# Kernel tuning notes

Measured on AMD Instinct MI355X. Metric: run time of the kernel, lower is better.

The kernel has to match this reference:

```python
import jax, jax.numpy as jnp
import numpy as np

# Config (matches init_kwargs / input_specs)
H = 128      # hidden_dim
D = 3        # depth (atom message-passing steps)
L = 2        # layers (molecule readout steps)
N = 100000   # total nodes in batch
E = 400000   # total directed edges
G = 5000     # number of graphs (molecules)
FN = 64      # num_atom_type
FE = 16      # num_bond_type


def setup_inputs() -> dict:
    key = jax.random.key(0)
    ks = jax.random.split(key, 32)
    rn = lambda k, shape, s=0.1: jax.random.normal(k, shape, jnp.float32) * s
    inp = {
        'node': rn(ks[0], (N, FN), 1.0),
        'edge': rn(ks[1], (E, FE), 1.0),
        'src': jax.random.randint(ks[2], (E,), 0, N),
        'dst': jax.random.randint(ks[3], (E,), 0, N),
        'graph_ids': jnp.sort(jax.random.randint(ks[4], (N,), 0, G)),
        # input embeddings
        'Wn0': rn(ks[5], (FN, H)), 'bn0': rn(ks[6], (H,)),
        'We0': rn(ks[7], (FE, H)), 'be0': rn(ks[8], (H,)),
        # Atom_AFPLayer params, stacked over depth D
        'aWn': rn(ks[9], (D, H, H)),      'abn': rn(ks[10], (D, H)),
        'aWe': rn(ks[11], (D, 2 * H, H)), 'abe': rn(ks[12], (D, H)),
        'aWal': rn(ks[13], (D, 2 * H, 1)),'abal': rn(ks[14], (D, 1)),
        'aWat': rn(ks[15], (D, H, H)),    'abat': rn(ks[16], (D, H)),
        'aWih': rn(ks[17], (D, H, 3 * H)),'abih': rn(ks[18], (D, 3 * H)),
        'aWhh': rn(ks[19], (D, H, 3 * H)),'abhh': rn(ks[20], (D, 3 * H)),
        # Mol_AFPLayer params, stacked over L
        'mWal': rn(ks[21], (L, 2 * H, 1)),'mbal': rn(ks[22], (L, 1)),
        'mWat': rn(ks[23], (L, H, H)),    'mbat': rn(ks[24], (L, H)),
        'mWih': rn(ks[25], (L, H, 3 * H)),'mbih': rn(ks[26], (L, 3 * H)),
        'mWhh': rn(ks[27], (L, H, 3 * H)),'mbhh': rn(ks[28], (L, 3 * H)),
        # final predictor
        'Wp': rn(ks[29], (H, 1)), 'bp': rn(ks[30], (1,)),
    }
    return inp


def _gru(x, h, Wih, bih, Whh, bhh):
    # torch.nn.GRUCell gate order: r, z, n
    gi = x @ Wih + bih
    gh = h @ Whh + bhh
    ir, iz, inn = jnp.split(gi, 3, axis=-1)
    hr, hz, hn = jnp.split(gh, 3, axis=-1)
    r = jax.nn.sigmoid(ir + hr)
    z = jax.nn.sigmoid(iz + hz)
    n = jnp.tanh(inn + r * hn)
    return (1.0 - z) * n + z * h


def _seg_softmax(score, seg, num):
    # numerically stable softmax within each segment; score: [E,1]
    m = jax.ops.segment_max(score, seg, num_segments=num)
    e = jnp.exp(score - m[seg])
    s = jax.ops.segment_sum(e, seg, num_segments=num)
    return e / s[seg]


def _forward(node, edge, src, dst, graph_ids,
             Wn0, bn0, We0, be0,
             aWn, abn, aWe, abe, aWal, abal, aWat, abat,
             aWih, abih, aWhh, abhh,
             mWal, mbal, mWat, mbat, mWih, mbih, mWhh, mbhh,
             Wp, bp):
    lrelu = jax.nn.leaky_relu  # slope 0.01, same as torch default
    n = lrelu(node @ Wn0 + bn0)   # [N,H] embedded nodes
    e = lrelu(edge @ We0 + be0)   # [E,H] embedded edges (constant across steps)
    Nn = n.shape[0]
    # Atom-level attentive message passing (depth D), per-layer weights
    for d in range(D):
        h = lrelu(n @ aWn[d] + abn[d])                                        # node_embedded_feats
        msg = lrelu(jnp.concatenate([h[src], e], -1) @ aWe[d] + abe[d])       # [E,H] neighbor_message
        score = lrelu(jnp.concatenate([msg, h[dst]], -1) @ aWal[d] + abal[d]) # [E,1]
        att = _seg_softmax(score, dst, Nn)                                    # edge_softmax over dst
        ctx = jax.ops.segment_sum(att * (msg @ aWat[d] + abat[d]), dst, num_segments=Nn)
        ctx = jax.nn.elu(ctx)
        n = jax.nn.relu(_gru(ctx, h, aWih[d], abih[d], aWhh[d], abhh[d]))
    # Molecule-level attentive readout (L steps)
    sn = jax.ops.segment_sum(n, graph_ids, num_segments=G)  # dgl.sum_nodes init
    for l in range(L):
        s = lrelu(sn)
        sc = lrelu(jnp.concatenate([n, s[graph_ids]], -1) @ mWal[l] + mbal[l])  # [N,1]
        aw = _seg_softmax(sc, graph_ids, G)                                     # softmax_nodes
        hid = n @ mWat[l] + mbat[l]
        sctx = jax.nn.elu(jax.ops.segment_sum(aw * hid, graph_ids, num_segments=G))
        sn = jax.nn.relu(_gru(sctx, s, mWih[l], mbih[l], mWhh[l], mbhh[l]))
    return sn @ Wp + bp  # [G,1]


def reference(node, edge, src, dst, graph_ids,
              Wn0, bn0, We0, be0,
              aWn, abn, aWe, abe, aWal, abal, aWat, abat,
              aWih, abih, aWhh, abhh,
              mWal, mbal, mWat, mbat, mWih, mbih, mWhh, mbhh,
              Wp, bp):
    return _forward(node, edge, src, dst, graph_ids,
                    Wn0, bn0, We0, be0,
                    aWn, abn, aWe, abe, aWal, abal, aWat, abat,
                    aWih, abih, aWhh, abhh,
                    mWal, mbal, mWat, mbat, mWih, mbih, mWhh, mbhh,
                    Wp, bp)
```

## Files before the change

### kernel.cpp

```cpp
#include <hip/hip_runtime.h>
#include <hip/hip_bf16.h>
#include <math.h>


#define HD 128
#define H3 384

typedef __attribute__((ext_vector_type(8))) short short8;
typedef __attribute__((ext_vector_type(4))) float f32x4;

__device__ __forceinline__ float lrelu_f(float x) { return x > 0.f ? x : 0.01f * x; }
__device__ __forceinline__ float sigmoid_f(float x) { return 1.f / (1.f + expf(-x)); }

__device__ __forceinline__ void atomicMaxF(float* addr, float val) {
    int iv = __float_as_int(val);
    if (iv >= 0) atomicMax((int*)addr, iv);
    else atomicMin((unsigned int*)addr, (unsigned int)iv);
}

__device__ __forceinline__ unsigned short bf16_rne(float v, float* back) {
    unsigned u = __float_as_uint(v);
    unsigned r = (u + 0x7FFFu + ((u >> 16) & 1u)) >> 16;
    *back = __uint_as_float(r << 16);
    return (unsigned short)r;
// ... 13 lines not shown
    float4 u0 = *reinterpret_cast<const float4*>(p);
    float4 u1 = *reinterpret_cast<const float4*>(p + 4);
    float vv[8] = {u0.x, u0.y, u0.z, u0.w, u1.x, u1.y, u1.z, u1.w};
#pragma unroll
    for (int j = 0; j < 8; ++j) {
        float back, d;
        h8[j] = (short)bf16_rne(vv[j], &back);
        l8[j] = (short)bf16_rne(vv[j] - back, &d);
    }
}

__device__ __forceinline__ void unpack8(const unsigned* p, short8& h8, short8& l8) {
    uint4 w0 = *reinterpret_cast<const uint4*>(p);
    uint4 w1 = *reinterpret_cast<const uint4*>(p + 4);
    unsigned ww[8] = {w0.x, w0.y, w0.z, w0.w, w1.x, w1.y, w1.z, w1.w};
#pragma unroll
    for (int j = 0; j < 8; ++j) {
        h8[j] = (short)(ww[j] >> 16);
        l8[j] = (short)(ww[j] & 0xffffu);
    }
}

__global__ void pack_b_kernel(const float* __restrict__ B, int K, int ldb, int col0,
                              int Ncols, short* __restrict__ hi, short* __restrict__ lo) {
    int KG = 4 * ((K + 31) / 32);
    int idx = blockIdx.x * blockDim.x + threadIdx.x;
    int total = (Ncols >> 4) * KG * 16;
    if (idx >= total) return;
    int col = idx & 15;
    int kg = (idx >> 4) % KG;
    int nblk = idx / (16 * KG);
    size_t o = (size_t)idx * 8;
#pragma unroll
    for (int e = 0; e < 8; ++e) {
        int k = kg * 8 + e;
        float v = (k < K) ? B[(size_t)k * ldb + col0 + nblk * 16 + col] : 0.f;
        float hf, d;
        unsigned short h = bf16_rne(v, &hf);
        unsigned short l = bf16_rne(v - hf, &d);
        hi[o + e] = (short)h;
        lo[o + e] = (short)l;
    }
}

__global__ __launch_bounds__(256) void mfma_gemm(
    const float* __restrict__ A, int K,
    const short* __restrict__ Bhi, const short* __restrict__ Blo, int KG,
    const float* __restrict__ bias, float* __restrict__ C, int M, int N, int act,
    const float* __restrict__ rdw, float* __restrict__ rdout,
    const float* __restrict__ rowmask, int outpk)
{
    const int t = threadIdx.x, lane = t & 63, w = t >> 6;
    const int wm = w & 1, wn = w >> 1, q = lane >> 4, r16 = lane & 15;
    const int m0 = blockIdx.x * 64, n0 = blockIdx.y * 64;
    const int KT = K >> 5;

    f32x4 acc[2][2];
#pragma unroll
    for (int a = 0; a < 2; ++a)
#pragma unroll
        for (int b = 0; b < 2; ++b) { acc[a][b][0]=0.f; acc[a][b][1]=0.f; acc[a][b][2]=0.f; acc[a][b][3]=0.f; }

    int arow[2];
#pragma unroll
    for (int mt = 0; mt < 2; ++mt) {
        int m = m0 + (wm << 5) + (mt << 4) + r16;
        arow[mt] = (m >= M) ? M - 1 : m;
    }

    for (int kt = 0; kt < KT; ++kt) {
        short8 ah[2], al[2];
#pragma unroll
        for (int mt = 0; mt < 2; ++mt)
            split8(A + (size_t)arow[mt] * K + (kt << 5) + (q << 3), ah[mt], al[mt]);
        const int kg = (kt << 2) + q;
#pragma unroll
        for (int nt = 0; nt < 2; ++nt) {
            int nblk = (n0 >> 4) + (wn << 1) + nt;
            size_t boff = (((size_t)nblk * KG + kg) * 16 + r16) * 8;
            short8 bh = *reinterpret_cast<const short8*>(Bhi + boff);
            short8 bl = *reinterpret_cast<const short8*>(Blo + boff);
#pragma unroll
            for (int mt = 0; mt < 2; ++mt) {
                acc[mt][nt] = __builtin_amdgcn_mfma_f32_16x16x32_bf16(ah[mt], bh, acc[mt][nt], 0, 0, 0);
                acc[mt][nt] = __builtin_amdgcn_mfma_f32_16x16x32_bf16(ah[mt], bl, acc[mt][nt], 0, 0, 0);
                acc[mt][nt] = __builtin_amdgcn_mfma_f32_16x16x32_bf16(al[mt], bh, acc[mt][nt], 0, 0, 0);
            }
        }
    }

#pragma unroll
    for (int mt = 0; mt < 2; ++mt) {
        float pv[4] = {0.f, 0.f, 0.f, 0.f};
#pragma unroll
        for (int nt = 0; nt < 2; ++nt) {
            int col = n0 + (wn << 5) + (nt << 4) + r16;
            float bi = bias ? bias[col] : 0.f;
// ... 7 lines not shown
                else if (act == 3) v = v > 0.f ? v : expf(v) - 1.f;
                if (rowmask && m < M && rowmask[m] == 0.f) v = 0.f;
                pv[i] += wc * v;
                if (m < M) {
                    if (outpk) ((unsigned*)C)[(size_t)m * N + col] = pack_hl(v);
                    else C[(size_t)m * N + col] = v;
                }
            }
        }
        if (rdw) {
#pragma unroll
            for (int i = 0; i < 4; ++i) {
                float p = pv[i];
                p += __shfl_xor(p, 1); p += __shfl_xor(p, 2);
                p += __shfl_xor(p, 4); p += __shfl_xor(p, 8);
                int m = m0 + (wm << 5) + (mt << 4) + (q << 2) + i;
                if (r16 == 0 && m < M) atomicAdd(&rdout[m], p);
            }
        }
    }
}

__global__ __launch_bounds__(256) void msg_pass_kernel(
    const unsigned* __restrict__ hpk, const int* __restrict__ src,
    const int* __restrict__ dst,
    const float* __restrict__ edge,
    const short* __restrict__ W0hi, const short* __restrict__ W0lo,
    const float* __restrict__ be0,
    const short* __restrict__ Wehi, const short* __restrict__ Welo,
    const float* __restrict__ be,
    const float* __restrict__ wal,
    float* __restrict__ sc, float* __restrict__ S,
    const int* __restrict__ ipos, void* __restrict__ msgpk, int fullprec,
    int E, int mode)
{
    __shared__ unsigned int elds[64 * 128];
    const int t = threadIdx.x, lane = t & 63, w = t >> 6;
    const int wm = w & 1, wn = w >> 1, q = lane >> 4, r16 = lane & 15;
    const int e0 = blockIdx.x * 64;

    {
        f32x4 ea[2][4];
#pragma unroll
        for (int a = 0; a < 2; ++a)
#pragma unroll
            for (int b = 0; b < 4; ++b) { ea[a][b][0]=0.f; ea[a][b][1]=0.f; ea[a][b][2]=0.f; ea[a][b][3]=0.f; }
        short8 eah[2], eal[2];
#pragma unroll
        for (int mt = 0; mt < 2; ++mt) {
            int er = e0 + (wm << 5) + (mt << 4) + r16;
            if (er >= E) er = E - 1;
            if (q < 2) split8(edge + (size_t)er * 16 + (q << 3), eah[mt], eal[mt]);
            else {
#pragma unroll
                for (int j = 0; j < 8; ++j) { eah[mt][j] = 0; eal[mt][j] = 0; }
            }
        }
#pragma unroll
        for (int nt = 0; nt < 4; ++nt) {
            int nblk = (wn << 2) + nt;
            size_t boff = (((size_t)nblk * 4 + q) * 16 + r16) * 8;
            short8 bh = *reinterpret_cast<const short8*>(W0hi + boff);
            short8 bl = *reinterpret_cast<const short8*>(W0lo + boff);
#pragma unroll
            for (int mt = 0; mt < 2; ++mt) {
                ea[mt][nt] = __builtin_amdgcn_mfma_f32_16x16x32_bf16(eah[mt], bh, ea[mt][nt], 0, 0, 0);
                ea[mt][nt] = __builtin_amdgcn_mfma_f32_16x16x32_bf16(eah[mt], bl, ea[mt][nt], 0, 0, 0);
                ea[mt][nt] = __builtin_amdgcn_mfma_f32_16x16x32_bf16(eal[mt], bh, ea[mt][nt], 0, 0, 0);
            }
        }
#pragma unroll
        for (int mt = 0; mt < 2; ++mt)
#pragma unroll
            for (int nt = 0; nt < 4; ++nt) {
                int col = (wn << 6) + (nt << 4) + r16;
#pragma unroll
                for (int i = 0; i < 4; ++i) {
                    int row = (wm << 5) + (mt << 4) + (q << 2) + i;
                    float v = lrelu_f(ea[mt][nt][i] + be0[col]);
                    elds[row * 128 + (col ^ ((row & 7) << 2))] = pack_hl(v);
                }
            }
    }
    __syncthreads();

    f32x4 acc[2][4];
#pragma unroll
    for (int a = 0; a < 2; ++a)
#pragma unroll
        for (int b = 0; b < 4; ++b) { acc[a][b][0]=0.f; acc[a][b][1]=0.f; acc[a][b][2]=0.f; acc[a][b][3]=0.f; }
    int grow[2], arw[2];
#pragma unroll
    for (int mt = 0; mt < 2; ++mt) {
        int m = e0 + (wm << 5) + (mt << 4) + r16;
        if (m >= E) m = E - 1;
        grow[mt] = src[m];
        arw[mt] = (wm << 5) + (mt << 4) + r16;
    }
#pragma unroll
    for (int kt = 0; kt < 8; ++kt) {
        short8 ah[2], al[2];
#pragma unroll
        for (int mt = 0; mt < 2; ++mt) {
            if (kt < 4) {
                unpack8(hpk + (size_t)grow[mt] * HD + (kt << 5) + (q << 3), ah[mt], al[mt]);
            } else {
                int row = arw[mt];
                int sh = (row & 7) << 2;
                int c = ((kt - 4) << 5) + (q << 3);
                uint4 w0 = *reinterpret_cast<const uint4*>(&elds[row * 128 + (c ^ sh)]);
                uint4 w1 = *reinterpret_cast<const uint4*>(&elds[row * 128 + ((c + 4) ^ sh)]);
                unsigned ww[8] = {w0.x, w0.y, w0.z, w0.w, w1.x, w1.y, w1.z, w1.w};
#pragma unroll
                for (int j = 0; j < 8; ++j) {
                    ah[mt][j] = (short)(ww[j] >> 16);
                    al[mt][j] = (short)(ww[j] & 0xffffu);
                }
            }
        }
// ... 1 lines not shown
#pragma unroll
        for (int nt = 0; nt < 4; ++nt) {
            int nblk = (wn << 2) + nt;
            size_t boff = (((size_t)nblk * 32 + kg) * 16 + r16) * 8;
            short8 bh = *reinterpret_cast<const short8*>(Wehi + boff);
            short8 bl = *reinterpret_cast<const short8*>(Welo + boff);
#pragma unroll
            for (int mt = 0; mt < 2; ++mt) {
                acc[mt][nt] = __builtin_amdgcn_mfma_f32_16x16x32_bf16(ah[mt], bh, acc[mt][nt], 0, 0, 0);
                acc[mt][nt] = __builtin_amdgcn_mfma_f32_16x16x32_bf16(ah[mt], bl, acc[mt][nt], 0, 0, 0);
                acc[mt][nt] = __builtin_amdgcn_mfma_f32_16x16x32_bf16(al[mt], bh, acc[mt][nt], 0, 0, 0);
            }
        }
    }

    if (mode == 2) {
#pragma unroll
        for (int mt = 0; mt < 2; ++mt)
#pragma unroll
            for (int i = 0; i < 4; ++i) {
                int m = e0 + (wm << 5) + (mt << 4) + (q << 2) + i;
                if (m >= E) continue;
                float a = sc[m];
                int dn = dst[m];
#pragma unroll
                for (int nt = 0; nt < 4; ++nt) {
                    int col = (wn << 6) + (nt << 4) + r16;
                    float v = lrelu_f(acc[mt][nt][i] + be[col]);
                    atomicAdd(&S[(size_t)dn * HD + col], a * v);
                }
            }
        return;
    }

#pragma unroll
    for (int mt = 0; mt < 2; ++mt) {
        float pv[4] = {0.f, 0.f, 0.f, 0.f};
#pragma unroll
        for (int i = 0; i < 4; ++i) {
            int m = e0 + (wm << 5) + (mt << 4) + (q << 2) + i;
            int ip = (mode == 0 && m < E) ? ipos[m] : 0;
#pragma unroll
            for (int nt = 0; nt < 4; ++nt) {
                int col = (wn << 6) + (nt << 4) + r16;
                float v = lrelu_f(acc[mt][nt][i] + be[col]);
                pv[i] += wal[col] * v;
                if (mode == 0 && m < E) {
                    size_t ro = (size_t)ip * HD + col;
                    if (fullprec) ((unsigned*)msgpk)[ro] = pack_hl(v);
                    else { float b_; ((unsigned short*)msgpk)[ro] = bf16_rne(v, &b_); }
                }
            }
        }
#pragma unroll
        for (int i = 0; i < 4; ++i) {
            float p = pv[i];
            p += __shfl_xor(p, 1); p += __shfl_xor(p, 2);
            p += __shfl_xor(p, 4); p += __shfl_xor(p, 8);
            int m = e0 + (wm << 5) + (mt << 4) + (q << 2) + i;
            if (r16 == 0 && m < E) atomicAdd(&sc[m], p);
        }
    }
}

__global__ __launch_bounds__(256) void ctx_gather_kernel(
    const void* __restrict__ msgpk, const float* __restrict__ sc,
    const int* __restrict__ csr, const int* __restrict__ rowptr,
    float* __restrict__ S, int Nn, int fullprec)
{
    int wid = (blockIdx.x * blockDim.x + threadIdx.x) >> 6;
    int lane = threadIdx.x & 63;
    if (wid >= Nn) return;
    int p0 = rowptr[wid], p1 = rowptr[wid + 1];
    float a0 = 0.f, a1 = 0.f;
    if (fullprec) {
        const unsigned* mp = (const unsigned*)msgpk;
        for (int p = p0; p < p1; ++p) {
            float a = sc[csr[p]];
            uint2 w = *reinterpret_cast<const uint2*>(mp + (size_t)p * HD + lane * 2);
            a0 += a * unpack_f32(w.x);
            a1 += a * unpack_f32(w.y);
        }
    } else {
        const unsigned short* mp = (const unsigned short*)msgpk;
        for (int p = p0; p < p1; ++p) {
            float a = sc[csr[p]];
            unsigned w = *reinterpret_cast<const unsigned*>(mp + (size_t)p * HD + lane * 2);
            a0 += a * __uint_as_float(w << 16);
            a1 += a * __uint_as_float(w & 0xffff0000u);
        }
    }
    S[(size_t)wid * HD + lane * 2] = a0;
    S[(size_t)wid * HD + lane * 2 + 1] = a1;
}

__global__ void hist_kernel(const int* __restrict__ dst, int* __restrict__ cnt, int E) {
    int i = blockIdx.x * blockDim.x + threadIdx.x;
    if (i < E) atomicAdd(&cnt[dst[i]], 1);
}
__global__ void scan1_kernel(const int* __restrict__ cnt, int* __restrict__ pre,
                             int* __restrict__ btot, int total) {
    __shared__ int ts[256];
    int base = blockIdx.x * 1024;
    int c[4], tsum = 0;
#pragma unroll
    for (int j = 0; j < 4; ++j) {
        int idx = base + threadIdx.x * 4 + j;
        c[j] = (idx < total) ? cnt[idx] : 0;
        tsum += c[j];
    }
    ts[threadIdx.x] = tsum;
    __syncthreads();
    for (int off = 1; off < 256; off <<= 1) {
        int v = (threadIdx.x >= off) ? ts[threadIdx.x - off] : 0;
        __syncthreads();
        ts[threadIdx.x] += v;
// ... 5 lines not shown
        int idx = base + threadIdx.x * 4 + j;
        if (idx < total) pre[idx] = run;
        run += c[j];
    }
    if (threadIdx.x == 255) btot[blockIdx.x] = ts[255];
}
__global__ void scan2_kernel(int* __restrict__ btot, int nb) {
    __shared__ int ts[256];
    int v = (threadIdx.x < nb) ? btot[threadIdx.x] : 0;
    ts[threadIdx.x] = v;
    __syncthreads();
    for (int off = 1; off < 256; off <<= 1) {
        int u = (threadIdx.x >= off) ? ts[threadIdx.x - off] : 0;
        __syncthreads();
        ts[threadIdx.x] += u;
        __syncthreads();
    }
    if (threadIdx.x < nb) btot[threadIdx.x] = ts[threadIdx.x] - v;
}
__global__ void scan3_kernel(int* __restrict__ pre, const int* __restrict__ btot, int total) {
    int i = blockIdx.x * blockDim.x + threadIdx.x;
    if (i < total) pre[i] += btot[i >> 10];
}
__global__ void fill_kernel(const int* __restrict__ dst, const int* __restrict__ rowptr,
                            int* __restrict__ fillc, int* __restrict__ csr,
                            int* __restrict__ ipos, int E) {
    int i = blockIdx.x * blockDim.x + threadIdx.x;
    if (i >= E) return;
    int d = dst[i];
    int pos = rowptr[d] + atomicAdd(&fillc[d], 1);
    csr[pos] = i;
    ipos[i] = pos;
}

#define GRU_SL (8 * 16 * 16 * 8)
__global__ __launch_bounds__(256) void gru_fused_kernel(
    const unsigned* __restrict__ ctxpk, const unsigned* __restrict__ hpk,
    const short* __restrict__ ghi, const short* __restrict__ glo,
    const float* __restrict__ bih, const float* __restrict__ bhh,
    float* __restrict__ out, int M)
{
    const int t = threadIdx.x, lane = t & 63, w = t >> 6;
    const int wm = w & 1, wn = w >> 1, q = lane >> 4, r16 = lane & 15;
    const int m0 = blockIdx.x * 64, j0 = blockIdx.y * 64;

    f32x4 acc[6][2][2];
#pragma unroll
    for (int g = 0; g < 6; ++g)
#pragma unroll
        for (int a = 0; a < 2; ++a)
#pragma unroll
            for (int b = 0; b < 2; ++b) { acc[g][a][b][0]=0.f; acc[g][a][b][1]=0.f; acc[g][a][b][2]=0.f; acc[g][a][b][3]=0.f; }

    int arow[2];
#pragma unroll
    for (int mt = 0; mt < 2; ++mt) {
        int m = m0 + (wm << 5) + (mt << 4) + r16;
        arow[mt] = (m >= M) ? M - 1 : m;
    }

#pragma unroll
    for (int kt = 0; kt < 4; ++kt) {
        short8 ah[2], al[2];
// ... 37 lines not shown
                    acc[g][mt][nt] = __builtin_amdgcn_mfma_f32_16x16x32_bf16(ah[mt], bh, acc[g][mt][nt], 0, 0, 0);
                    acc[g][mt][nt] = __builtin_amdgcn_mfma_f32_16x16x32_bf16(ah[mt], bl, acc[g][mt][nt], 0, 0, 0);
                    acc[g][mt][nt] = __builtin_amdgcn_mfma_f32_16x16x32_bf16(al[mt], bh, acc[g][mt][nt], 0, 0, 0);
                }
            }
    }

#pragma unroll
    for (int mt = 0; mt < 2; ++mt)
#pragma unroll
        for (int nt = 0; nt < 2; ++nt) {
            int j = j0 + (wn << 5) + (nt << 4) + r16;
            float bir = bih[j], biz = bih[HD + j], bin = bih[2 * HD + j];
            float bhr = bhh[j], bhz = bhh[HD + j], bhn = bhh[2 * HD + j];
#pragma unroll
            for (int i = 0; i < 4; ++i) {
                int m = m0 + (wm << 5) + (mt << 4) + (q << 2) + i;
                if (m >= M) continue;
                float r = sigmoid_f(acc[0][mt][nt][i] + bir + acc[3][mt][nt][i] + bhr);
                float z = sigmoid_f(acc[1][mt][nt][i] + biz + acc[4][mt][nt][i] + bhz);
                float hn = acc[5][mt][nt][i] + bhn;
                float nn = tanhf(acc[2][mt][nt][i] + bin + r * hn);
                float hv = unpack_f32(hpk[(size_t)m * HD + j]);
                out[(size_t)m * HD + j] = fmaxf((1.f - z) * nn + z * hv, 0.f);
            }
        }
}

__global__ void init_maxsum_kernel(float* mx, float* sm, int n) {
    int i = blockIdx.x * blockDim.x + threadIdx.x;
    if (i < n) { mx[i] = -__builtin_inff(); sm[i] = 0.f; }
}

__global__ void score_combine_kernel(float* __restrict__ sc, const float* __restrict__ hd2,
                                     const int* __restrict__ seg, const float* __restrict__ bal,
                                     float* __restrict__ maxbuf, int count) {
    int i = blockIdx.x * blockDim.x + threadIdx.x;
    if (i >= count) return;
    int s = seg[i];
    float v = lrelu_f(sc[i] + hd2[s] + bal[0]);
    sc[i] = v;
    atomicMaxF(&maxbuf[s], v);
}

__global__ __launch_bounds__(256) void score_kernel(
    const float* __restrict__ A, const float* __restrict__ B,
    const int* __restrict__ seg, const float* __restrict__ w,
    const float* __restrict__ bal, float* __restrict__ out,
    float* __restrict__ maxbuf, int count)
{
    int i = (blockIdx.x * blockDim.x + threadIdx.x) >> 6;
    int lane = threadIdx.x & 63;
    if (i >= count) return;
    int s = seg[i];
    const float* ar = A + (size_t)i * HD;
    const float* br = B + (size_t)s * HD;
    float p = ar[lane] * w[lane] + ar[lane + 64] * w[lane + 64]
            + br[lane] * w[128 + lane] + br[lane + 64] * w[192 + lane];
#pragma unroll
    for (int off = 32; off > 0; off >>= 1) p += __shfl_down(p, off);
    if (lane == 0) {
        float v = lrelu_f(p + bal[0]);
        out[i] = v;
        atomicMaxF(&maxbuf[s], v);
    }
}

__global__ void expsum_kernel(float* __restrict__ sc, const float* __restrict__ mx,
                              float* __restrict__ sm, const int* __restrict__ seg, int count) {
    int i = blockIdx.x * blockDim.x + threadIdx.x;
    if (i >= count) return;
    int s = seg[i];
    float p = expf(sc[i] - mx[s]);
    sc[i] = p;
    atomicAdd(&sm[s], p);
}

__global__ void attdiv_kernel(float* __restrict__ sc, const float* __restrict__ sm,
                              const int* __restrict__ seg, int count) {
    int i = blockIdx.x * blockDim.x + threadIdx.x;
// ... 1 lines not shown
    sc[i] = sc[i] / sm[seg[i]];
}

__global__ void gru_gate_kernel(const float* __restrict__ gi, const float* __restrict__ gh,
                                const float* __restrict__ h, float* __restrict__ out, int M) {
    size_t idx = (size_t)blockIdx.x * blockDim.x + threadIdx.x;
    if (idx >= (size_t)M * HD) return;
    size_t row = idx >> 7; int col = (int)(idx & 127);
    const float* gir = gi + row * H3;
    const float* ghr = gh + row * H3;
    float r = sigmoid_f(gir[col] + ghr[col]);
    float z = sigmoid_f(gir[col + 128] + ghr[col + 128]);
    float nn = tanhf(gir[col + 256] + r * ghr[col + 256]);
    float o = (1.f - z) * nn + z * h[idx];
    out[idx] = fmaxf(o, 0.f);
}

__global__ void lrelu_copy_kernel(const float* __restrict__ in, float* __restrict__ out, size_t n) {
    size_t i = (size_t)blockIdx.x * blockDim.x + threadIdx.x;
    if (i >= n) return;
    out[i] = lrelu_f(in[i]);
}

__global__ void segsum_kernel(const float* __restrict__ nb, const int* __restrict__ gid,
                              float* __restrict__ sn, int Nn) {
    size_t idx = (size_t)blockIdx.x * blockDim.x + threadIdx.x;
    if (idx >= (size_t)Nn * HD) return;
    size_t row = idx >> 7; int col = (int)(idx & 127);
    atomicAdd(&sn[(size_t)gid[row] * HD + col], nb[idx]);
}

__global__ void seg_scale_sum_kernel(const float* __restrict__ nb, const int* __restrict__ gid,
                                     const float* __restrict__ scale, float* __restrict__ out, int Nn) {
    size_t idx = (size_t)blockIdx.x * blockDim.x + threadIdx.x;
    if (idx >= (size_t)Nn * HD) return;
    size_t row = idx >> 7; int col = (int)(idx & 127);
    atomicAdd(&out[(size_t)gid[row] * HD + col], scale[row] * nb[idx]);
}

__global__ void final_kernel(const float* __restrict__ sn, const float* __restrict__ Wp,
                             const float* __restrict__ bp, float* __restrict__ out, int G) {
    int g = (blockIdx.x * blockDim.x + threadIdx.x) >> 6;
    int lane = threadIdx.x & 63;
    if (g >= G) return;
    const float* r = sn + (size_t)g * HD;
    float p = r[lane] * Wp[lane] + r[lane + 64] * Wp[lane + 64];
#pragma unroll
    for (int off = 32; off > 0; off >>= 1) p += __shfl_down(p, off);
    if (lane == 0) out[g] = p + bp[0];
}

__global__ void canary_kernel(float* out, int n) {
    int i = blockIdx.x * blockDim.x + threadIdx.x;
    if (i < n) out[i] = 123.456f;
}

struct PkB { const short* hi; const short* lo; int KG; };

extern "C" void kernel_launch(void* const* d_in, const int* in_sizes, int n_in,
                              void* d_out, int out_size, void* d_ws, size_t ws_size,
// ... 20 lines not shown
    const float* aWhh = (const float*)d_in[19];
    const float* abhh = (const float*)d_in[20];
    const float* mWal = (const float*)d_in[21];
    const float* mbal = (const float*)d_in[22];
    const float* mWat = (const float*)d_in[23];
    const float* mbat = (const float*)d_in[24];
    const float* mWih = (const float*)d_in[25];
    const float* mbih = (const float*)d_in[26];
    const float* mWhh = (const float*)d_in[27];
    const float* mbhh = (const float*)d_in[28];
    const float* Wp   = (const float*)d_in[29];
    const float* bp   = (const float*)d_in[30];

    const int N = in_sizes[0] / 64;
    const int E = in_sizes[1] / 16;
    const int G = out_size;
    const int D = in_sizes[9] / (HD * HD);
    const int L = in_sizes[21] / (2 * HD);
    if (D > 8 || L > 4) return;

    char* wsb = (char*)d_ws;

    short* pkcur = (short*)wsb;
    auto packB = [&](const float* B, int K, int ldb, int col0, int Ncols) -> PkB {
        int KG = 4 * ((K + 31) / 32);
        size_t elems = (size_t)(Ncols >> 4) * KG * 16 * 8;
        short* hi = pkcur; pkcur += elems;
        short* lo = pkcur; pkcur += elems;
        int total = (Ncols >> 4) * KG * 16;
        pack_b_kernel<<<(total + 255) / 256, 256, 0, stream>>>(B, K, ldb, col0, Ncols, hi, lo);
        PkB p; p.hi = hi; p.lo = lo; p.KG = KG; return p;
    };
    PkB pWe0 = packB(We0, 16, HD, 0, HD);
    PkB pWn0 = packB(Wn0, 64, HD, 0, HD);
    PkB pAWn[8], pAWe[8], pAWat[8];
    const short *gHi[8], *gLo[8];
    for (int d = 0; d < D; ++d) {
        pAWn[d]  = packB(aWn  + (size_t)d * HD * HD,     HD,     HD, 0, HD);
        pAWe[d]  = packB(aWe  + (size_t)d * 2 * HD * HD, 2 * HD, HD, 0, HD);
        pAWat[d] = packB(aWat + (size_t)d * HD * HD,     HD,     HD, 0, HD);
        short* ghi = pkcur; pkcur += 6 * GRU_SL;
        short* glo = pkcur; pkcur += 6 * GRU_SL;
        for (int g = 0; g < 3; ++g) {
            int total = (HD >> 4) * 16 * 16;
            pack_b_kernel<<<(total + 255) / 256, 256, 0, stream>>>(
                aWih + (size_t)d * HD * H3, HD, H3, g * HD, HD, ghi + g * GRU_SL, glo + g * GRU_SL);
            pack_b_kernel<<<(total + 255) / 256, 256, 0, stream>>>(
                aWhh + (size_t)d * HD * H3, HD, H3, g * HD, HD, ghi + (3 + g) * GRU_SL, glo + (3 + g) * GRU_SL);
        }
        gHi[d] = ghi; gLo[d] = glo;
    }
    PkB pMWat[4], pMWih[4], pMWhh[4];
    for (int l = 0; l < L; ++l) {
        pMWat[l] = packB(mWat + (size_t)l * HD * HD, HD, HD, 0, HD);
        pMWih[l] = packB(mWih + (size_t)l * HD * H3, HD, H3, 0, H3);
        pMWhh[l] = packB(mWhh + (size_t)l * HD * H3, HD, H3, 0, H3);
    }

    size_t off = ((size_t)((char*)pkcur - wsb) + 255) & ~(size_t)255;
    auto alloc = [&](size_t bytes) -> void* {
        void* p = (void*)(wsb + off);
        off += (bytes + 255) & ~(size_t)255;
        return p;
    };
    float*    nbuf  = (float*)alloc((size_t)N * HD * 4);
    unsigned* hpk   = (unsigned*)alloc((size_t)N * HD * 4);
    float* sc_e = (float*)alloc((size_t)E * 4);
    float* nmax = (float*)alloc((size_t)N * 4);
    float* nsum = (float*)alloc((size_t)N * 4);
    float* sc_n = (float*)alloc((size_t)N * 4);
    float* hd2  = (float*)alloc((size_t)N * 4);
    float* sn   = (float*)alloc((size_t)G * HD * 4);
    float* gmax = (float*)alloc((size_t)G * 4);
    float* gsum = (float*)alloc((size_t)G * 4);
    int* cnt    = (int*)alloc((size_t)(N + 1) * 4);
    int* rowptr = (int*)alloc((size_t)(N + 1) * 4);
    int* fillc  = (int*)alloc((size_t)N * 4);
    int* csr    = (int*)alloc((size_t)E * 4);
    int* ipos   = (int*)alloc((size_t)E * 4);
    int* btot   = (int*)alloc(1024 * 4);

    size_t ovr_off = off;
    size_t ctx_bytes = (size_t)N * HD * 4;
    size_t mol_bytes = 3 * ((size_t)G * HD * 4 + 256) + 2 * ((size_t)G * H3 * 4 + 256);
    size_t min_ovr = ctx_bytes > mol_bytes ? ctx_bytes : mol_bytes;
    int csr_mode, fullprec = 0;
    size_t mf = (size_t)E * HD * 4, mh = (size_t)E * HD * 2;
    if (ovr_off + (mf > min_ovr ? mf : min_ovr) <= ws_size) { csr_mode = 1; fullprec = 1; }
    else if (ovr_off + (mh > min_ovr ? mh : min_ovr) <= ws_size) { csr_mode = 1; fullprec = 0; }
    else if (ovr_off + min_ovr <= ws_size) { csr_mode = 0; }
    else {
        canary_kernel<<<(G + 255) / 256, 256, 0, stream>>>((float*)d_out, G);
        return;
    }
    void*     msgpk = (void*)(wsb + ovr_off);
    unsigned* ctxpk = (unsigned*)(wsb + ovr_off);
    size_t mo = ovr_off;
    auto molalloc = [&](size_t bytes) -> float* {
        float* p = (float*)(wsb + mo);
        mo += (bytes + 255) & ~(size_t)255;
        return p;
    };
    float* sbuf = molalloc((size_t)G * HD * 4);
    float* sctx = molalloc((size_t)G * HD * 4);
    float* Sg   = molalloc((size_t)G * HD * 4);
    float* gim  = molalloc((size_t)G * H3 * 4);
    float* ghm  = molalloc((size_t)G * H3 * 4);

    const int total_sc = N + 1;
    const int nb = (total_sc + 1023) / 1024;
    if (csr_mode && nb > 256) csr_mode = 0;

    auto mgemm = [&](const float* A, int K, const PkB& pk, const float* bias, void* C,
                     int M, int Nc, int act, const float* rdw, float* rdout,
                     const float* rowmask, int outpk) {
        dim3 g((M + 63) / 64, Nc / 64);
        mfma_gemm<<<g, dim3(256), 0, stream>>>(A, K, pk.hi, pk.lo, pk.KG, bias, (float*)C,
                                               M, Nc, act, rdw, rdout, rowmask, outpk);
    };

    if (csr_mode) {
        hipMemsetAsync(cnt, 0, (size_t)(N + 1) * 4, stream);
        hipMemsetAsync(fillc, 0, (size_t)N * 4, stream);
        hist_kernel<<<(E + 255) / 256, 256, 0, stream>>>(dst, cnt, E);
        scan1_kernel<<<nb, 256, 0, stream>>>(cnt, rowptr, btot, total_sc);
        scan2_kernel<<<1, 256, 0, stream>>>(btot, nb);
        scan3_kernel<<<(total_sc + 255) / 256, 256, 0, stream>>>(rowptr, btot, total_sc);
        fill_kernel<<<(E + 255) / 256, 256, 0, stream>>>(dst, rowptr, fillc, csr, ipos, E);
    }

    mgemm(node, 64, pWn0, bn0, nbuf, N, HD, 1, nullptr, nullptr, nullptr, 0);

    const int EB = (E + 63) / 64;
    for (int d = 0; d < D; ++d) {
        const float* bn_d  = abn  + (size_t)d * HD;
        const float* be_d  = abe  + (size_t)d * HD;
        const float* Wal_d = aWal + (size_t)d * 2 * HD;
        const float* bal_d = abal + d;
        const float* bat_d = abat + (size_t)d * HD;
        const float* bih_d = abih + (size_t)d * H3;
        const float* bhh_d = abhh + (size_t)d * H3;

        hipMemsetAsync(hd2, 0, (size_t)N * 4, stream);
        hipMemsetAsync(sc_e, 0, (size_t)E * 4, stream);
        mgemm(nbuf, HD, pAWn[d], bn_d, hpk, N, HD, 1, Wal_d + HD, hd2, nullptr, 1);
        init_maxsum_kernel<<<(N + 255) / 256, 256, 0, stream>>>(nmax, nsum, N);
        msg_pass_kernel<<<EB, 256, 0, stream>>>(hpk, src, dst, edge, pWe0.hi, pWe0.lo, be0,
                                                pAWe[d].hi, pAWe[d].lo, be_d, Wal_d,
                                                sc_e, nullptr, ipos, msgpk, fullprec, E,
                                                csr_mode ? 0 : 1);
        score_combine_kernel<<<(E + 255) / 256, 256, 0, stream>>>(sc_e, hd2, dst, bal_d, nmax, E);
        expsum_kernel<<<(E + 255) / 256, 256, 0, stream>>>(sc_e, nmax, nsum, dst, E);
        attdiv_kernel<<<(E + 255) / 256, 256, 0, stream>>>(sc_e, nsum, dst, E);
        if (csr_mode) {
            ctx_gather_kernel<<<(N + 3) / 4, 256, 0, stream>>>(msgpk, sc_e, csr, rowptr,
                                                               nbuf, N, fullprec);
        } else {
            hipMemsetAsync(nbuf, 0, (size_t)N * HD * 4, stream);
            msg_pass_kernel<<<EB, 256, 0, stream>>>(hpk, src, dst, edge, pWe0.hi, pWe0.lo, be0,
                                                    pAWe[d].hi, pAWe[d].lo, be_d, nullptr,
                                                    sc_e, nbuf, nullptr, nullptr, 0, E, 2);
        }
        mgemm(nbuf, HD, pAWat[d], bat_d, ctxpk, N, HD, 3, nullptr, nullptr, nsum, 1);
        dim3 gg((N + 63) / 64, 2);
        gru_fused_kernel<<<gg, dim3(256), 0, stream>>>(ctxpk, hpk, gHi[d], gLo[d],
                                                       bih_d, bhh_d, nbuf, N);
    }

    hipMemsetAsync(sn, 0, (size_t)G * HD * 4, stream);
    segsum_kernel<<<((size_t)N * HD + 255) / 256, 256, 0, stream>>>(nbuf, gid, sn, N);
    for (int l = 0; l < L; ++l) {
        const float* Wal_l = mWal + (size_t)l * 2 * HD;
        const float* bal_l = mbal + l;
        const float* bat_l = mbat + (size_t)l * HD;
        const float* bih_l = mbih + (size_t)l * H3;
        const float* bhh_l = mbhh + (size_t)l * H3;

        lrelu_copy_kernel<<<((size_t)G * HD + 255) / 256, 256, 0, stream>>>(sn, sbuf, (size_t)G * HD);
        init_maxsum_kernel<<<(G + 255) / 256, 256, 0, stream>>>(gmax, gsum, G);
        score_kernel<<<(N + 3) / 4, 256, 0, stream>>>(nbuf, sbuf, gid, Wal_l, bal_l, sc_n, gmax, N);
        expsum_kernel<<<(N + 255) / 256, 256, 0, stream>>>(sc_n, gmax, gsum, gid, N);
        attdiv_kernel<<<(N + 255) / 256, 256, 0, stream>>>(sc_n, gsum, gid, N);
        hipMemsetAsync(Sg, 0, (size_t)G * HD * 4, stream);
        seg_scale_sum_kernel<<<((size_t)N * HD + 255) / 256, 256, 0, stream>>>(nbuf, gid, sc_n, Sg, N);
        mgemm(Sg, HD, pMWat[l], bat_l, sctx, G, HD, 3, nullptr, nullptr, gsum, 0);
        mgemm(sctx, HD, pMWih[l], bih_l, gim, G, H3, 0, nullptr, nullptr, nullptr, 0);
        mgemm(sbuf, HD, pMWhh[l], bhh_l, ghm, G, H3, 0, nullptr, nullptr, nullptr, 0);
        gru_gate_kernel<<<((size_t)G * HD + 255) / 256, 256, 0, stream>>>(gim, ghm, sbuf, sn, G);
    }

    final_kernel<<<(G + 3) / 4, 256, 0, stream>>>(sn, Wp, bp, (float*)d_out, G);
}
```

Baseline: 2.108 ms.

## Sort edges by destination and store node features pre-split as packed bf16 hi/lo

Edges are now permuted into dst-sorted order up front, and src, dst and edge ids are stored in that order. This lets msg_pass write messages and ctx_gather read attention scores contiguously without the csr/ipos indirection. Node feature buffers are stored as packed hi/lo bf16 words, so GEMMs unpack them instead of re-splitting fp32 each time. Weight packing for stacked matrices is batched into fewer launches. The permuted edge-feature reads become gathers, and the non-CSR fallback now writes fp32 atomics into a buffer typed as packed while the GEMM reads it as fp32.

After: 1.845 ms. 12.5% less time.

```diff
diff --git a/kernel.cpp b/kernel.cpp
--- a/kernel.cpp
+++ b/kernel.cpp
@@ -59,8 +59,13 @@
 }
 
 __global__ void pack_b_kernel(const float* __restrict__ B, int K, int ldb, int col0,
-                              int Ncols, short* __restrict__ hi, short* __restrict__ lo) {
+                              int Ncols, short* __restrict__ hi, short* __restrict__ lo,
+                              size_t matB, size_t matO) {
     int KG = 4 * ((K + 31) / 32);
+    int mat = blockIdx.y;
+    B += (size_t)mat * matB;
+    hi += (size_t)mat * matO;
+    lo += (size_t)mat * matO;
     int idx = blockIdx.x * blockDim.x + threadIdx.x;
     int total = (Ncols >> 4) * KG * 16;
     if (idx >= total) return;
@@ -80,12 +85,40 @@
     }
 }
 
+#define GRU_SL (8 * 16 * 16 * 8)
+__global__ void pack_gru_kernel(const float* __restrict__ Wih, const float* __restrict__ Whh,
+                                int D, short* __restrict__ hi, short* __restrict__ lo) {
+    const int per = 6 * (GRU_SL / 8);
+    int idx = blockIdx.x * blockDim.x + threadIdx.x;
+    if (idx >= D * per) return;
+    int d = idx / per;
+    int r = idx % per;
+    int s = r / (GRU_SL / 8);
+    int g8 = r % (GRU_SL / 8);
+    int col = g8 & 15;
+    int kg = (g8 >> 4) & 15;
+    int nblk = g8 >> 8;
+    const float* B = (s < 3 ? Wih : Whh) + (size_t)d * HD * H3;
+    int col0 = (s % 3) * HD;
+    size_t o = (size_t)idx * 8;
+#pragma unroll
+    for (int e = 0; e < 8; ++e) {
+        int k = kg * 8 + e;
+        float v = B[(size_t)k * H3 + col0 + nblk * 16 + col];
+        float hf, d2;
+        unsigned short h = bf16_rne(v, &hf);
+        unsigned short l = bf16_rne(v - hf, &d2);
+        hi[o + e] = (short)h;
+        lo[o + e] = (short)l;
+    }
+}
+
 __global__ __launch_bounds__(256) void mfma_gemm(
     const float* __restrict__ A, int K,
     const short* __restrict__ Bhi, const short* __restrict__ Blo, int KG,
     const float* __restrict__ bias, float* __restrict__ C, int M, int N, int act,
     const float* __restrict__ rdw, float* __restrict__ rdout,
-    const float* __restrict__ rowmask, int outpk)
+    const float* __restrict__ rowmask, int outpk, int apk)
 {
     const int t = threadIdx.x, lane = t & 63, w = t >> 6;
     const int wm = w & 1, wn = w >> 1, q = lane >> 4, r16 = lane & 15;
@@ -108,8 +141,11 @@
     for (int kt = 0; kt < KT; ++kt) {
         short8 ah[2], al[2];
 #pragma unroll
-        for (int mt = 0; mt < 2; ++mt)
-            split8(A + (size_t)arow[mt] * K + (kt << 5) + (q << 3), ah[mt], al[mt]);
+        for (int mt = 0; mt < 2; ++mt) {
+            size_t aoff = (size_t)arow[mt] * K + (kt << 5) + (q << 3);
+            if (apk) unpack8((const unsigned*)A + aoff, ah[mt], al[mt]);
+            else split8(A + aoff, ah[mt], al[mt]);
+        }
         const int kg = (kt << 2) + q;
 #pragma unroll
         for (int nt = 0; nt < 2; ++nt) {
@@ -163,8 +199,8 @@
 }
 
 __global__ __launch_bounds__(256) void msg_pass_kernel(
-    const unsigned* __restrict__ hpk, const int* __restrict__ src,
-    const int* __restrict__ dst,
+    const unsigned* __restrict__ hpk, const int* __restrict__ srcp,
+    const int* __restrict__ dstp, const int* __restrict__ eidp,
     const float* __restrict__ edge,
     const short* __restrict__ W0hi, const short* __restrict__ W0lo,
     const float* __restrict__ be0,
@@ -172,7 +208,7 @@
     const float* __restrict__ be,
     const float* __restrict__ wal,
     float* __restrict__ sc, float* __restrict__ S,
-    const int* __restrict__ ipos, void* __restrict__ msgpk, int fullprec,
+    void* __restrict__ msgpk, int fullprec,
     int E, int mode)
 {
     __shared__ unsigned int elds[64 * 128];
@@ -191,7 +227,8 @@
         for (int mt = 0; mt < 2; ++mt) {
             int er = e0 + (wm << 5) + (mt << 4) + r16;
             if (er >= E) er = E - 1;
-            if (q < 2) split8(edge + (size_t)er * 16 + (q << 3), eah[mt], eal[mt]);
+            int eid = eidp[er];
+            if (q < 2) split8(edge + (size_t)eid * 16 + (q << 3), eah[mt], eal[mt]);
             else {
 #pragma unroll
                 for (int j = 0; j < 8; ++j) { eah[mt][j] = 0; eal[mt][j] = 0; }
@@ -235,7 +272,7 @@
     for (int mt = 0; mt < 2; ++mt) {
         int m = e0 + (wm << 5) + (mt << 4) + r16;
         if (m >= E) m = E - 1;
-        grow[mt] = src[m];
+        grow[mt] = srcp[m];
         arw[mt] = (wm << 5) + (mt << 4) + r16;
     }
 #pragma unroll
@@ -283,7 +320,7 @@
                 int m = e0 + (wm << 5) + (mt << 4) + (q << 2) + i;
                 if (m >= E) continue;
                 float a = sc[m];
-                int dn = dst[m];
+                int dn = dstp[m];
 #pragma unroll
                 for (int nt = 0; nt < 4; ++nt) {
                     int col = (wn << 6) + (nt << 4) + r16;
@@ -300,14 +337,13 @@
 #pragma unroll
         for (int i = 0; i < 4; ++i) {
             int m = e0 + (wm << 5) + (mt << 4) + (q << 2) + i;
-            int ip = (mode == 0 && m < E) ? ipos[m] : 0;
 #pragma unroll
             for (int nt = 0; nt < 4; ++nt) {
                 int col = (wn << 6) + (nt << 4) + r16;
                 float v = lrelu_f(acc[mt][nt][i] + be[col]);
                 pv[i] += wal[col] * v;
                 if (mode == 0 && m < E) {
-                    size_t ro = (size_t)ip * HD + col;
+                    size_t ro = (size_t)m * HD + col;
                     if (fullprec) ((unsigned*)msgpk)[ro] = pack_hl(v);
                     else { float b_; ((unsigned short*)msgpk)[ro] = bf16_rne(v, &b_); }
                 }
@@ -326,8 +362,7 @@
 
 __global__ __launch_bounds__(256) void ctx_gather_kernel(
     const void* __restrict__ msgpk, const float* __restrict__ sc,
-    const int* __restrict__ csr, const int* __restrict__ rowptr,
-    float* __restrict__ S, int Nn, int fullprec)
+    const int* __restrict__ rowptr, unsigned* __restrict__ Spk, int Nn, int fullprec)
 {
     int wid = (blockIdx.x * blockDim.x + threadIdx.x) >> 6;
     int lane = threadIdx.x & 63;
@@ -337,7 +372,7 @@
     if (fullprec) {
         const unsigned* mp = (const unsigned*)msgpk;
         for (int p = p0; p < p1; ++p) {
-            float a = sc[csr[p]];
+            float a = sc[p];
             uint2 w = *reinterpret_cast<const uint2*>(mp + (size_t)p * HD + lane * 2);
             a0 += a * unpack_f32(w.x);
             a1 += a * unpack_f32(w.y);
@@ -345,14 +380,14 @@
     } else {
         const unsigned short* mp = (const unsigned short*)msgpk;
         for (int p = p0; p < p1; ++p) {
-            float a = sc[csr[p]];
+            float a = sc[p];
             unsigned w = *reinterpret_cast<const unsigned*>(mp + (size_t)p * HD + lane * 2);
             a0 += a * __uint_as_float(w << 16);
             a1 += a * __uint_as_float(w & 0xffff0000u);
         }
     }
-    S[(size_t)wid * HD + lane * 2] = a0;
-    S[(size_t)wid * HD + lane * 2 + 1] = a1;
+    Spk[(size_t)wid * HD + lane * 2] = pack_hl(a0);
+    Spk[(size_t)wid * HD + lane * 2 + 1] = pack_hl(a1);
 }
 
 __global__ void hist_kernel(const int* __restrict__ dst, int* __restrict__ cnt, int E) {
@@ -404,23 +439,24 @@
     int i = blockIdx.x * blockDim.x + threadIdx.x;
     if (i < total) pre[i] += btot[i >> 10];
 }
-__global__ void fill_kernel(const int* __restrict__ dst, const int* __restrict__ rowptr,
-                            int* __restrict__ fillc, int* __restrict__ csr,
-                            int* __restrict__ ipos, int E) {
+__global__ void fill_kernel(const int* __restrict__ src, const int* __restrict__ dst,
+                            const int* __restrict__ rowptr, int* __restrict__ fillc,
+                            int* __restrict__ srcp, int* __restrict__ dstp,
+                            int* __restrict__ eidp, int E) {
     int i = blockIdx.x * blockDim.x + threadIdx.x;
     if (i >= E) return;
     int d = dst[i];
     int pos = rowptr[d] + atomicAdd(&fillc[d], 1);
-    csr[pos] = i;
-    ipos[i] = pos;
-}
-
-#define GRU_SL (8 * 16 * 16 * 8)
+    srcp[pos] = src[i];
+    dstp[pos] = d;
+    eidp[pos] = i;
+}
+
 __global__ __launch_bounds__(256) void gru_fused_kernel(
     const unsigned* __restrict__ ctxpk, const unsigned* __restrict__ hpk,
     const short* __restrict__ ghi, const short* __restrict__ glo,
     const float* __restrict__ bih, const float* __restrict__ bhh,
-    float* __restrict__ out, int M)
+    unsigned* __restrict__ out, int M)
 {
     const int t = threadIdx.x, lane = t & 63, w = t >> 6;
     const int wm = w & 1, wn = w >> 1, q = lane >> 4, r16 = lane & 15;
@@ -504,7 +540,7 @@
                 float hn = acc[5][mt][nt][i] + bhn;
                 float nn = tanhf(acc[2][mt][nt][i] + bin + r * hn);
                 float hv = unpack_f32(hpk[(size_t)m * HD + j]);
-                out[(size_t)m * HD + j] = fmaxf((1.f - z) * nn + z * hv, 0.f);
+                out[(size_t)m * HD + j] = pack_hl(fmaxf((1.f - z) * nn + z * hv, 0.f));
             }
         }
 }
@@ -526,7 +562,7 @@
 }
 
 __global__ __launch_bounds__(256) void score_kernel(
-    const float* __restrict__ A, const float* __restrict__ B,
+    const unsigned* __restrict__ Apk, const float* __restrict__ B,
     const int* __restrict__ seg, const float* __restrict__ w,
     const float* __restrict__ bal, float* __restrict__ out,
     float* __restrict__ maxbuf, int count)
@@ -535,9 +571,10 @@
     int lane = threadIdx.x & 63;
     if (i >= count) return;
     int s = seg[i];
-    const float* ar = A + (size_t)i * HD;
+    float a0 = unpack_f32(Apk[(size_t)i * HD + lane]);
+    float a1 = unpack_f32(Apk[(size_t)i * HD + lane + 64]);
     const float* br = B + (size_t)s * HD;
-    float p = ar[lane] * w[lane] + ar[lane + 64] * w[lane + 64]
+    float p = a0 * w[lane] + a1 * w[lane + 64]
             + br[lane] * w[128 + lane] + br[lane + 64] * w[192 + lane];
 #pragma unroll
     for (int off = 32; off > 0; off >>= 1) p += __shfl_down(p, off);
@@ -585,20 +622,20 @@
     out[i] = lrelu_f(in[i]);
 }
 
-__global__ void segsum_kernel(const float* __restrict__ nb, const int* __restrict__ gid,
+__global__ void segsum_kernel(const unsigned* __restrict__ npk, const int* __restrict__ gid,
                               float* __restrict__ sn, int Nn) {
     size_t idx = (size_t)blockIdx.x * blockDim.x + threadIdx.x;
     if (idx >= (size_t)Nn * HD) return;
     size_t row = idx >> 7; int col = (int)(idx & 127);
-    atomicAdd(&sn[(size_t)gid[row] * HD + col], nb[idx]);
-}
-
-__global__ void seg_scale_sum_kernel(const float* __restrict__ nb, const int* __restrict__ gid,
+    atomicAdd(&sn[(size_t)gid[row] * HD + col], unpack_f32(npk[idx]));
+}
+
+__global__ void seg_scale_sum_kernel(const unsigned* __restrict__ npk, const int* __restrict__ gid,
                                      const float* __restrict__ scale, float* __restrict__ out, int Nn) {
     size_t idx = (size_t)blockIdx.x * blockDim.x + threadIdx.x;
     if (idx >= (size_t)Nn * HD) return;
     size_t row = idx >> 7; int col = (int)(idx & 127);
-    atomicAdd(&out[(size_t)gid[row] * HD + col], scale[row] * nb[idx]);
+    atomicAdd(&out[(size_t)gid[row] * HD + col], scale[row] * unpack_f32(npk[idx]));
 }
 
 __global__ void final_kernel(const float* __restrict__ sn, const float* __restrict__ Wp,
@@ -665,39 +702,49 @@
     char* wsb = (char*)d_ws;
 
     short* pkcur = (short*)wsb;
-    auto packB = [&](const float* B, int K, int ldb, int col0, int Ncols) -> PkB {
+    size_t elN;
+    auto packBn = [&](const float* B, int K, int ldb, int col0, int Ncols,
+                      int nmat, size_t matB) -> PkB {
         int KG = 4 * ((K + 31) / 32);
         size_t elems = (size_t)(Ncols >> 4) * KG * 16 * 8;
-        short* hi = pkcur; pkcur += elems;
-        short* lo = pkcur; pkcur += elems;
+        elN = elems;
+        short* hi = pkcur; pkcur += elems * nmat;
+        short* lo = pkcur; pkcur += elems * nmat;
         int total = (Ncols >> 4) * KG * 16;
-        pack_b_kernel<<<(total + 255) / 256, 256, 0, stream>>>(B, K, ldb, col0, Ncols, hi, lo);
+        dim3 g((total + 255) / 256, nmat);
+        pack_b_kernel<<<g, 256, 0, stream>>>(B, K, ldb, col0, Ncols, hi, lo, matB, elems);
         PkB p; p.hi = hi; p.lo = lo; p.KG = KG; return p;
     };
-    PkB pWe0 = packB(We0, 16, HD, 0, HD);
-    PkB pWn0 = packB(Wn0, 64, HD, 0, HD);
+    PkB pWe0 = packBn(We0, 16, HD, 0, HD, 1, 0);
+    PkB pWn0 = packBn(Wn0, 64, HD, 0, HD, 1, 0);
     PkB pAWn[8], pAWe[8], pAWat[8];
+    {
+        PkB b = packBn(aWn, HD, HD, 0, HD, D, (size_t)HD * HD);
+        for (int d = 0; d < D; ++d) { pAWn[d] = b; pAWn[d].hi = b.hi + d * elN; pAWn[d].lo = b.lo + d * elN; }
+        b = packBn(aWe, 2 * HD, HD, 0, HD, D, (size_t)2 * HD * HD);
+        for (int d = 0; d < D; ++d) { pAWe[d] = b; pAWe[d].hi = b.hi + d * elN; pAWe[d].lo = b.lo + d * elN; }
+        b = packBn(aWat, HD, HD, 0, HD, D, (size_t)HD * HD);
+        for (int d = 0; d < D; ++d) { pAWat[d] = b; pAWat[d].hi = b.hi + d * elN; pAWat[d].lo = b.lo + d * elN; }
+    }
+    short* ghiAll = pkcur; pkcur += (size_t)D * 6 * GRU_SL;
+    short* gloAll = pkcur; pkcur += (size_t)D * 6 * GRU_SL;
+    {
+        int total = D * 6 * (GRU_SL / 8);
+        pack_gru_kernel<<<(total + 255) / 256, 256, 0, stream>>>(aWih, aWhh, D, ghiAll, gloAll);
+    }
     const short *gHi[8], *gLo[8];
     for (int d = 0; d < D; ++d) {
-        pAWn[d]  = packB(aWn  + (size_t)d * HD * HD,     HD,     HD, 0, HD);
-        pAWe[d]  = packB(aWe  + (size_t)d * 2 * HD * HD, 2 * HD, HD, 0, HD);
-        pAWat[d] = packB(aWat + (size_t)d * HD * HD,     HD,     HD, 0, HD);
-        short* ghi = pkcur; pkcur += 6 * GRU_SL;
-        short* glo = pkcur; pkcur += 6 * GRU_SL;
-        for (int g = 0; g < 3; ++g) {
-            int total = (HD >> 4) * 16 * 16;
-            pack_b_kernel<<<(total + 255) / 256, 256, 0, stream>>>(
-                aWih + (size_t)d * HD * H3, HD, H3, g * HD, HD, ghi + g * GRU_SL, glo + g * GRU_SL);
-            pack_b_kernel<<<(total + 255) / 256, 256, 0, stream>>>(
-                aWhh + (size_t)d * HD * H3, HD, H3, g * HD, HD, ghi + (3 + g) * GRU_SL, glo + (3 + g) * GRU_SL);
-        }
-        gHi[d] = ghi; gLo[d] = glo;
+        gHi[d] = ghiAll + (size_t)d * 6 * GRU_SL;
+        gLo[d] = gloAll + (size_t)d * 6 * GRU_SL;
     }
     PkB pMWat[4], pMWih[4], pMWhh[4];
-    for (int l = 0; l < L; ++l) {
-        pMWat[l] = packB(mWat + (size_t)l * HD * HD, HD, HD, 0, HD);
-        pMWih[l] = packB(mWih + (size_t)l * HD * H3, HD, H3, 0, H3);
-        pMWhh[l] = packB(mWhh + (size_t)l * HD * H3, HD, H3, 0, H3);
+    {
+        PkB b = packBn(mWat, HD, HD, 0, HD, L, (size_t)HD * HD);
+        for (int l = 0; l < L; ++l) { pMWat[l] = b; pMWat[l].hi = b.hi + l * elN; pMWat[l].lo = b.lo + l * elN; }
+        b = packBn(mWih, HD, H3, 0, H3, L, (size_t)HD * H3);
+        for (int l = 0; l < L; ++l) { pMWih[l] = b; pMWih[l].hi = b.hi + l * elN; pMWih[l].lo = b.lo + l * elN; }
+        b = packBn(mWhh, HD, H3, 0, H3, L, (size_t)HD * H3);
+        for (int l = 0; l < L; ++l) { pMWhh[l] = b; pMWhh[l].hi = b.hi + l * elN; pMWhh[l].lo = b.lo + l * elN; }
     }
 
     size_t off = ((size_t)((char*)pkcur - wsb) + 255) & ~(size_t)255;
@@ -706,8 +753,8 @@
         off += (bytes + 255) & ~(size_t)255;
         return p;
     };
-    float*    nbuf  = (float*)alloc((size_t)N * HD * 4);
-    unsigned* hpk   = (unsigned*)alloc((size_t)N * HD * 4);
+    unsigned* npk = (unsigned*)alloc((size_t)N * HD * 4);
+    unsigned* hpk = (unsigned*)alloc((size_t)N * HD * 4);
     float* sc_e = (float*)alloc((size_t)E * 4);
     float* nmax = (float*)alloc((size_t)N * 4);
     float* nsum = (float*)alloc((size_t)N * 4);
@@ -719,8 +766,9 @@
     int* cnt    = (int*)alloc((size_t)(N + 1) * 4);
     int* rowptr = (int*)alloc((size_t)(N + 1) * 4);
     int* fillc  = (int*)alloc((size_t)N * 4);
-    int* csr    = (int*)alloc((size_t)E * 4);
-    int* ipos   = (int*)alloc((size_t)E * 4);
+    int* srcp   = (int*)alloc((size_t)E * 4);
+    int* dstp   = (int*)alloc((size_t)E * 4);
+    int* eidp   = (int*)alloc((size_t)E * 4);
     int* btot   = (int*)alloc(1024 * 4);
 
     size_t ovr_off = off;
@@ -752,27 +800,30 @@
 
     const int total_sc = N + 1;
     const int nb = (total_sc + 1023) / 1024;
-    if (csr_mode && nb > 256) csr_mode = 0;
-
-    auto mgemm = [&](const float* A, int K, const PkB& pk, const float* bias, void* C,
+    if (nb > 256) {
+        canary_kernel<<<(G + 255) / 256, 256, 0, stream>>>((float*)d_out, G);
+        return;
+    }
+
+    auto mgemm = [&](const void* A, int K, const PkB& pk, const float* bias, void* C,
                      int M, int Nc, int act, const float* rdw, float* rdout,
-                     const float* rowmask, int outpk) {
+                     const float* rowmask, int outpk, int apk) {
         dim3 g((M + 63) / 64, Nc / 64);
-        mfma_gemm<<<g, dim3(256), 0, stream>>>(A, K, pk.hi, pk.lo, pk.KG, bias, (float*)C,
-                                               M, Nc, act, rdw, rdout, rowmask, outpk);
+        mfma_gemm<<<g, dim3(256), 0, stream>>>((const float*)A, K, pk.hi, pk.lo, pk.KG,
+                                               bias, (float*)C, M, Nc, act, rdw, rdout,
+                                               rowmask, outpk, apk);
     };
 
-    if (csr_mode) {
-        hipMemsetAsync(cnt, 0, (size_t)(N + 1) * 4, stream);
-        hipMemsetAsync(fillc, 0, (size_t)N * 4, stream);
-        hist_kernel<<<(E + 255) / 256, 256, 0, stream>>>(dst, cnt, E);
-        scan1_kernel<<<nb, 256, 0, stream>>>(cnt, rowptr, btot, total_sc);
-        scan2_kernel<<<1, 256, 0, stream>>>(btot, nb);
-        scan3_kernel<<<(total_sc + 255) / 256, 256, 0, stream>>>(rowptr, btot, total_sc);
-        fill_kernel<<<(E + 255) / 256, 256, 0, stream>>>(dst, rowptr, fillc, csr, ipos, E);
-    }
-
-    mgemm(node, 64, pWn0, bn0, nbuf, N, HD, 1, nullptr, nullptr, nullptr, 0);
+    hipMemsetAsync(cnt, 0, (size_t)(N + 1) * 4, stream);
+    hipMemsetAsync(fillc, 0, (size_t)N * 4, stream);
+    hist_kernel<<<(E + 255) / 256, 256, 0, stream>>>(dst, cnt, E);
+    scan1_kernel<<<nb, 256, 0, stream>>>(cnt, rowptr, btot, total_sc);
+    scan2_kernel<<<1, 256, 0, stream>>>(btot, nb);
+    scan3_kernel<<<(total_sc + 255) / 256, 256, 0, stream>>>(rowptr, btot, total_sc);
+    fill_kernel<<<(E + 255) / 256, 256, 0, stream>>>(src, dst, rowptr, fillc,
+                                                     srcp, dstp, eidp, E);
+
+    mgemm(node, 64, pWn0, bn0, npk, N, HD, 1, nullptr, nullptr, nullptr, 1, 0);
 
     const int EB = (E + 63) / 64;
     for (int d = 0; d < D; ++d) {
@@ -786,32 +837,35 @@
 
         hipMemsetAsync(hd2, 0, (size_t)N * 4, stream);
         hipMemsetAsync(sc_e, 0, (size_t)E * 4, stream);
-        mgemm(nbuf, HD, pAWn[d], bn_d, hpk, N, HD, 1, Wal_d + HD, hd2, nullptr, 1);
+        mgemm(npk, HD, pAWn[d], bn_d, hpk, N, HD, 1, Wal_d + HD, hd2, nullptr, 1, 1);
         init_maxsum_kernel<<<(N + 255) / 256, 256, 0, stream>>>(nmax, nsum, N);
-        msg_pass_kernel<<<EB, 256, 0, stream>>>(hpk, src, dst, edge, pWe0.hi, pWe0.lo, be0,
+        msg_pass_kernel<<<EB, 256, 0, stream>>>(hpk, srcp, dstp, eidp, edge,
+                                                pWe0.hi, pWe0.lo, be0,
                                                 pAWe[d].hi, pAWe[d].lo, be_d, Wal_d,
-                                                sc_e, nullptr, ipos, msgpk, fullprec, E,
+                                                sc_e, nullptr, msgpk, fullprec, E,
                                                 csr_mode ? 0 : 1);
-        score_combine_kernel<<<(E + 255) / 256, 256, 0, stream>>>(sc_e, hd2, dst, bal_d, nmax, E);
-        expsum_kernel<<<(E + 255) / 256, 256, 0, stream>>>(sc_e, nmax, nsum, dst, E);
-        attdiv_kernel<<<(E + 255) / 256, 256, 0, stream>>>(sc_e, nsum, dst, E);
+        score_combine_kernel<<<(E + 255) / 256, 256, 0, stream>>>(sc_e, hd2, dstp, bal_d, nmax, E);
+        expsum_kernel<<<(E + 255) / 256, 256, 0, stream>>>(sc_e, nmax, nsum, dstp, E);
+        attdiv_kernel<<<(E + 255) / 256, 256, 0, stream>>>(sc_e, nsum, dstp, E);
         if (csr_mode) {
-            ctx_gather_kernel<<<(N + 3) / 4, 256, 0, stream>>>(msgpk, sc_e, csr, rowptr,
-                                                               nbuf, N, fullprec);
+            ctx_gather_kernel<<<(N + 3) / 4, 256, 0, stream>>>(msgpk, sc_e, rowptr,
+                                                               npk, N, fullprec);
         } else {
-            hipMemsetAsync(nbuf, 0, (size_t)N * HD * 4, stream);
-            msg_pass_kernel<<<EB, 256, 0, stream>>>(hpk, src, dst, edge, pWe0.hi, pWe0.lo, be0,
+            hipMemsetAsync(npk, 0, (size_t)N * HD * 4, stream);
+            msg_pass_kernel<<<EB, 256, 0, stream>>>(hpk, srcp, dstp, eidp, edge,
+                                                    pWe0.hi, pWe0.lo, be0,
                                                     pAWe[d].hi, pAWe[d].lo, be_d, nullptr,
-                                                    sc_e, nbuf, nullptr, nullptr, 0, E, 2);
-        }
-        mgemm(nbuf, HD, pAWat[d], bat_d, ctxpk, N, HD, 3, nullptr, nullptr, nsum, 1);
+                                                    sc_e, (float*)npk, nullptr, 0, E, 2);
+        }
+        mgemm(npk, HD, pAWat[d], bat_d, ctxpk, N, HD, 3, nullptr, nullptr, nsum, 1,
+              csr_mode ? 1 : 0);
         dim3 gg((N + 63) / 64, 2);
         gru_fused_kernel<<<gg, dim3(256), 0, stream>>>(ctxpk, hpk, gHi[d], gLo[d],
-                                                       bih_d, bhh_d, nbuf, N);
+                                                       bih_d, bhh_d, npk, N);
     }
 
     hipMemsetAsync(sn, 0, (size_t)G * HD * 4, stream);
-    segsum_kernel<<<((size_t)N * HD + 255) / 256, 256, 0, stream>>>(nbuf, gid, sn, N);
+    segsum_kernel<<<((size_t)N * HD + 255) / 256, 256, 0, stream>>>(npk, gid, sn, N);
     for (int l = 0; l < L; ++l) {
         const float* Wal_l = mWal + (size_t)l * 2 * HD;
         const float* bal_l = mbal + l;
@@ -821,14 +875,14 @@
 
         lrelu_copy_kernel<<<((size_t)G * HD + 255) / 256, 256, 0, stream>>>(sn, sbuf, (size_t)G * HD);
         init_maxsum_kernel<<<(G + 255) / 256, 256, 0, stream>>>(gmax, gsum, G);
-        score_kernel<<<(N + 3) / 4, 256, 0, stream>>>(nbuf, sbuf, gid, Wal_l, bal_l, sc_n, gmax, N);
+        score_kernel<<<(N + 3) / 4, 256, 0, stream>>>(npk, sbuf, gid, Wal_l, bal_l, sc_n, gmax, N);
         expsum_kernel<<<(N + 255) / 256, 256, 0, stream>>>(sc_n, gmax, gsum, gid, N);
         attdiv_kernel<<<(N + 255) / 256, 256, 0, stream>>>(sc_n, gsum, gid, N);
         hipMemsetAsync(Sg, 0, (size_t)G * HD * 4, stream);
-        seg_scale_sum_kernel<<<((size_t)N * HD + 255) / 256, 256, 0, stream>>>(nbuf, gid, sc_n, Sg, N);
-        mgemm(Sg, HD, pMWat[l], bat_l, sctx, G, HD, 3, nullptr, nullptr, gsum, 0);
-        mgemm(sctx, HD, pMWih[l], bih_l, gim, G, H3, 0, nullptr, nullptr, nullptr, 0);
-        mgemm(sbuf, HD, pMWhh[l], bhh_l, ghm, G, H3, 0, nullptr, nullptr, nullptr, 0);
+        seg_scale_sum_kernel<<<((size_t)N * HD + 255) / 256, 256, 0, stream>>>(npk, gid, sc_n, Sg, N);
+        mgemm(Sg, HD, pMWat[l], bat_l, sctx, G, HD, 3, nullptr, nullptr, gsum, 0, 0);
+        mgemm(sctx, HD, pMWih[l], bih_l, gim, G, H3, 0, nullptr, nullptr, nullptr, 0, 0);
+        mgemm(sbuf, HD, pMWhh[l], bhh_l, ghm, G, H3, 0, nullptr, nullptr, nullptr, 0, 0);
         gru_gate_kernel<<<((size_t)G * HD + 255) / 256, 256, 0, stream>>>(gim, ghm, sbuf, sn, G);
     }
 
```
